# Optimization experiments

Measured on AMD Instinct MI355X. Metric: run time of the kernel, lower is better.

The kernel has to match this reference:

```python
import jax, jax.numpy as jnp
import numpy as np

N_NODES = 100000
N_EDGES = 1600000
IN_FEATS = 128
HIDDEN = 128
N_CLASSES = 47


def setup_inputs() -> dict:
    key = jax.random.key(0)
    ks = jax.random.split(key, 8)
    x = jax.random.normal(ks[0], (N_NODES, IN_FEATS), dtype=jnp.float32)
    edges = jax.random.randint(ks[1], (2, N_EDGES), 0, N_NODES, dtype=jnp.int32)
    W0 = jax.random.normal(ks[2], (IN_FEATS, HIDDEN), dtype=jnp.float32) * (1.0 / np.sqrt(IN_FEATS))
    b0 = jnp.zeros((HIDDEN,), dtype=jnp.float32)
    W1 = jax.random.normal(ks[3], (HIDDEN, HIDDEN), dtype=jnp.float32) * (1.0 / np.sqrt(HIDDEN))
    b1 = jnp.zeros((HIDDEN,), dtype=jnp.float32)
    Wc = jax.random.normal(ks[4], (HIDDEN, N_CLASSES), dtype=jnp.float32) * (1.0 / np.sqrt(HIDDEN))
    bc = jnp.zeros((N_CLASSES,), dtype=jnp.float32)
    return {"x": x, "edges": edges, "W0": W0, "b0": b0, "W1": W1, "b1": b1, "Wc": Wc, "bc": bc}


def reference(x, edges, W0, b0, W1, b1, Wc, bc):
    N = x.shape[0]
    src, dst = edges[0], edges[1]
    ones = jnp.ones((src.shape[0],), dtype=x.dtype)
    # symmetric 'both' normalization: out-degree for src, in-degree for dst (clamped to >=1)
    out_deg = jax.ops.segment_sum(ones, src, num_segments=N)
    in_deg = jax.ops.segment_sum(ones, dst, num_segments=N)
    c_src = jnp.maximum(out_deg, 1.0) ** -0.5  # [N]
    c_dst = jnp.maximum(in_deg, 1.0) ** -0.5   # [N]

    def graph_conv(h, W, b):
        h = (h * c_src[:, None]) @ W                       # dense transform [N, H]
        h = jax.ops.segment_sum(h[src], dst, num_segments=N)  # sparse SpMM aggregation
        h = h * c_dst[:, None] + b
        return jax.nn.relu(h)

    h = graph_conv(x, W0, b0)
    h = graph_conv(h, W1, b1)
    return h @ Wc + bc
```

## Files before the change

### kernel.cpp

```cpp
#include <hip/hip_runtime.h>
#include <hip/hip_fp16.h>


#define PB 256
#define BSHIFT 8

typedef _Float16 f16x8 __attribute__((ext_vector_type(8)));
typedef float f32x4 __attribute__((ext_vector_type(4)));


__global__ __launch_bounds__(256) void k_count(const int* __restrict__ src, const int* __restrict__ dst,
                                               int E, int per_blk, int NB,
                                               int* __restrict__ cntT, int* __restrict__ cntT2) {
  __shared__ int cnt[512];
  __shared__ int cnt2[512];
  for (int i = threadIdx.x; i < 512; i += 256) { cnt[i] = 0; cnt2[i] = 0; }
  __syncthreads();
  int e0 = blockIdx.x * per_blk, e1 = min(E, e0 + per_blk);
  for (int e = e0 + threadIdx.x; e < e1; e += 256) {
    atomicAdd(&cnt[dst[e] >> BSHIFT], 1);
    atomicAdd(&cnt2[src[e] >> BSHIFT], 1);
  }
  __syncthreads();
  for (int i = threadIdx.x; i < NB; i += 256) {
    cntT[i * PB + blockIdx.x] = cnt[i];
    cntT2[i * PB + blockIdx.x] = cnt2[i];
  }
}

__global__ __launch_bounds__(256) void k_scanblk(const int* __restrict__ cntT, int* __restrict__ offsT,
                                                 int* __restrict__ total) {
  __shared__ int s[256];
  int b = blockIdx.x, t = threadIdx.x;
  int v = cntT[b * PB + t];
  s[t] = v;
  __syncthreads();
  for (int off = 1; off < 256; off <<= 1) {
    int x = (t >= off) ? s[t - off] : 0;
    __syncthreads();
    s[t] += x;
    __syncthreads();
  }
  offsT[b * PB + t] = s[t] - v;
  if (t == 255) total[b] = s[255];
}

__global__ __launch_bounds__(512) void k_scantot(const int* __restrict__ total, int NB, int E,
                                                 int* __restrict__ bbase, int* __restrict__ sbase,
                                                 int* __restrict__ row_ptr, int N) {
  __shared__ int s[512];
  int t = threadIdx.x;
  const int* tot = (blockIdx.x == 0) ? total : total + NB;
  int* obase = (blockIdx.x == 0) ? bbase : sbase;
  int v = (t < NB) ? tot[t] : 0;
  s[t] = v;
  __syncthreads();
  for (int off = 1; off < 512; off <<= 1) {
    int x = (t >= off) ? s[t - off] : 0;
    __syncthreads();
    s[t] += x;
    __syncthreads();
  }
  if (t < NB) obase[t] = s[t] - v;
  if (t == 0) obase[NB] = E;
  if (blockIdx.x == 0 && t == 0) row_ptr[N] = E;
}


__global__ __launch_bounds__(256) void k_partition(const int* __restrict__ src, const int* __restrict__ dst,
                                                   int E, int per_blk, int NB,
                                                   const int* __restrict__ offsT, const int* __restrict__ bbase,
                                                   const int* __restrict__ offsT2, const int* __restrict__ sbase,
                                                   unsigned* __restrict__ ebuf, unsigned char* __restrict__ sbuf,
                                                   int src_bits) {
  __shared__ int cur[512];
  __shared__ int cur2[512];
  for (int i = threadIdx.x; i < NB; i += 256) {
    cur[i] = bbase[i] + offsT[i * PB + blockIdx.x];
    cur2[i] = sbase[i] + offsT2[i * PB + blockIdx.x];
  }
  __syncthreads();
  int e0 = blockIdx.x * per_blk, e1 = min(E, e0 + per_blk);
  for (int e = e0 + threadIdx.x; e < e1; e += 256) {
    int d = dst[e], s = src[e];
    int pos = atomicAdd(&cur[d >> BSHIFT], 1);
    ebuf[pos] = ((unsigned)(d & ((1 << BSHIFT) - 1)) << src_bits) | (unsigned)s;
    int pos2 = atomicAdd(&cur2[s >> BSHIFT], 1);
    sbuf[pos2] = (unsigned char)(s & ((1 << BSHIFT) - 1));
  }
}


__global__ __launch_bounds__(256) void k_finalize_src(const unsigned char* __restrict__ sbuf,
                                                      const int* __restrict__ sbase, int N,
                                                      float* __restrict__ c_src) {
  __shared__ int cnt[256];
  int b = blockIdx.x, t = threadIdx.x;
  cnt[t] = 0;
  __syncthreads();
  int q0 = sbase[b], q1 = sbase[b + 1];
  for (int i = q0 + t; i < q1; i += 256) atomicAdd(&cnt[sbuf[i]], 1);
  __syncthreads();
  int node = (b << BSHIFT) + t;
  if (node < N) c_src[node] = rsqrtf((float)max(cnt[t], 1));
}


__global__ __launch_bounds__(256) void k_fin_gemm(const unsigned* __restrict__ ebuf, const int* __restrict__ bbase,
                                                  int N, int src_bits, int NB,
                                                  int* __restrict__ row_ptr, float* __restrict__ c_dst,
                                                  int* __restrict__ col_idx,
                                                  const float* __restrict__ A, const float* __restrict__ W,
                                                  const float* __restrict__ scale, __half* __restrict__ out) {
  __shared__ _Float16 Wt[128][136];
  int t = threadIdx.x;

  if (blockIdx.x < NB) {
    int* cnt = (int*)&Wt[0][0];
    int* s = cnt + 256;
    int* cur = cnt + 512;
    int b = blockIdx.x;
    int r0 = bbase[b], r1 = bbase[b + 1];
    cnt[t] = 0;
    __syncthreads();
    for (int i = r0 + t; i < r1; i += 256) atomicAdd(&cnt[ebuf[i] >> src_bits], 1);
    __syncthreads();
    int v = cnt[t];
    s[t] = v;
    __syncthreads();
    for (int off = 1; off < 256; off <<= 1) {
      int x = (t >= off) ? s[t - off] : 0;
      __syncthreads();
      s[t] += x;
      __syncthreads();
    }
    int ex = s[t] - v;
    cur[t] = ex;
    int node = (b << BSHIFT) + t;
    if (node < N) {
      row_ptr[node] = r0 + ex;
      c_dst[node] = rsqrtf((float)max(v, 1));
    }
    __syncthreads();
    unsigned smask = (1u << src_bits) - 1u;
    for (int i = r0 + t; i < r1; i += 256) {
      unsigned e = ebuf[i];
      int pos = r0 + atomicAdd(&cur[e >> src_bits], 1);
      col_idx[pos] = (int)((e & smask) << 8);
    }
    return;
  }

  int bid = blockIdx.x - NB;
  {
    int nlow = t & 15;
    int kplow = t >> 4;
#pragma unroll
    for (int j = 0; j < 32; j++) {
      int n = nlow + 16 * (j & 7);
      int kp = kplow + 16 * (j >> 3);
      float w0 = W[(size_t)(2 * kp) * 128 + n];
      float w1 = W[(size_t)(2 * kp + 1) * 128 + n];
      __half2 h2 = __floats2half2_rn(w0, w1);
      *(__half2*)&Wt[n][2 * kp] = h2;
    }
  }
  __syncthreads();

  int wave = t >> 6;
  int lane = t & 63;
  int li = lane & 15;
  int q = lane >> 4;

#pragma unroll
  for (int s2 = 0; s2 < 2; s2++) {
    int m0 = (bid * 2 + s2) * 128 + wave * 32;
    if (m0 >= N) break;

    int mrow[2];
    float csc[2];
    bool mok[2];
    const float* arow[2];
#pragma unroll
    for (int s = 0; s < 2; s++) {
      mrow[s] = m0 + s * 16 + li;
      mok[s] = mrow[s] < N;
      csc[s] = mok[s] ? scale[mrow[s]] : 0.f;
      arow[s] = A + (size_t)(mok[s] ? mrow[s] : 0) * 128;
    }

    f32x4 acc[2][8];
#pragma unroll
    for (int s = 0; s < 2; s++)
#pragma unroll
      for (int nt = 0; nt < 8; nt++) acc[s][nt] = (f32x4){0.f, 0.f, 0.f, 0.f};

#pragma unroll
    for (int kc = 0; kc < 128; kc += 32) {
      f16x8 af[2];
#pragma unroll
      for (int s = 0; s < 2; s++) {
        float4 a0 = *(const float4*)(arow[s] + kc + q * 8);
        float4 a1 = *(const float4*)(arow[s] + kc + q * 8 + 4);
        f16x8 v;
        v[0] = (_Float16)(a0.x * csc[s]);
        v[1] = (_Float16)(a0.y * csc[s]);
        v[2] = (_Float16)(a0.z * csc[s]);
        v[3] = (_Float16)(a0.w * csc[s]);
        v[4] = (_Float16)(a1.x * csc[s]);
        v[5] = (_Float16)(a1.y * csc[s]);
        v[6] = (_Float16)(a1.z * csc[s]);
        v[7] = (_Float16)(a1.w * csc[s]);
        af[s] = v;
      }
#pragma unroll
      for (int nt = 0; nt < 8; nt++) {
        f16x8 wf = *(const f16x8*)&Wt[nt * 16 + li][kc + q * 8];
        acc[0][nt] = __builtin_amdgcn_mfma_f32_16x16x32_f16(wf, af[0], acc[0][nt], 0, 0, 0);
        acc[1][nt] = __builtin_amdgcn_mfma_f32_16x16x32_f16(wf, af[1], acc[1][nt], 0, 0, 0);
      }
    }

#pragma unroll
    for (int s = 0; s < 2; s++) {
      if (!mok[s]) continue;
      size_t rb = (size_t)mrow[s] * 128;
#pragma unroll
      for (int nt = 0; nt < 8; nt++) {
        __half2 p0 = __floats2half2_rn(acc[s][nt][0], acc[s][nt][1]);
        __half2 p1 = __floats2half2_rn(acc[s][nt][2], acc[s][nt][3]);
        uint2 qv;
        qv.x = *(unsigned*)&p0;
        qv.y = *(unsigned*)&p1;
        *(uint2*)&out[rb + nt * 16 + q * 4] = qv;
      }
    }
  }
}


__device__ __forceinline__ f16x8 load_af(const __half* arow, int off, float csc) {
  f16x8 v = *(const f16x8*)(arow + off);
  _Float16 c = (_Float16)csc;
#pragma unroll
  for (int j = 0; j < 8; j++) v[j] = v[j] * c;
  return v;
}

__global__ __launch_bounds__(256) void k_gemm_mfma_h(const __half* __restrict__ A, const float* __restrict__ W,
                                                     const float* __restrict__ scale, __half* __restrict__ out, int N) {
  __shared__ _Float16 Wt[128][136];
  int t = threadIdx.x;
  {
    int nlow = t & 15;
    int kplow = t >> 4;
#pragma unroll
    for (int j = 0; j < 32; j++) {
      int n = nlow + 16 * (j & 7);
      int kp = kplow + 16 * (j >> 3);
      float w0 = W[(size_t)(2 * kp) * 128 + n];
      float w1 = W[(size_t)(2 * kp + 1) * 128 + n];
      __half2 h2 = __floats2half2_rn(w0, w1);
      *(__half2*)&Wt[n][2 * kp] = h2;
    }
  }
  __syncthreads();

  int wave = t >> 6;
  int lane = t & 63;
  int li = lane & 15;
  int q = lane >> 4;

#pragma unroll
  for (int s2 = 0; s2 < 2; s2++) {
    int m0 = (blockIdx.x * 2 + s2) * 128 + wave * 32;
    if (m0 >= N) break;

    int mrow[2];
    float csc[2];
    bool mok[2];
    const __half* arow[2];
#pragma unroll
    for (int s = 0; s < 2; s++) {
      mrow[s] = m0 + s * 16 + li;
      mok[s] = mrow[s] < N;
      csc[s] = mok[s] ? scale[mrow[s]] : 0.f;
      arow[s] = A + (size_t)(mok[s] ? mrow[s] : 0) * 128;
    }

    f32x4 acc[2][8];
#pragma unroll
    for (int s = 0; s < 2; s++)
#pragma unroll
      for (int nt = 0; nt < 8; nt++) acc[s][nt] = (f32x4){0.f, 0.f, 0.f, 0.f};

#pragma unroll
    for (int kc = 0; kc < 128; kc += 32) {
      f16x8 af[2];
#pragma unroll
      for (int s = 0; s < 2; s++) af[s] = load_af(arow[s], kc + q * 8, csc[s]);
#pragma unroll
      for (int nt = 0; nt < 8; nt++) {
        f16x8 wf = *(const f16x8*)&Wt[nt * 16 + li][kc + q * 8];
        acc[0][nt] = __builtin_amdgcn_mfma_f32_16x16x32_f16(wf, af[0], acc[0][nt], 0, 0, 0);
        acc[1][nt] = __builtin_amdgcn_mfma_f32_16x16x32_f16(wf, af[1], acc[1][nt], 0, 0, 0);
      }
    }

#pragma unroll
    for (int s = 0; s < 2; s++) {
      if (!mok[s]) continue;
      size_t rb = (size_t)mrow[s] * 128;
#pragma unroll
      for (int nt = 0; nt < 8; nt++) {
        __half2 p0 = __floats2half2_rn(acc[s][nt][0], acc[s][nt][1]);
        __half2 p1 = __floats2half2_rn(acc[s][nt][2], acc[s][nt][3]);
        uint2 qv;
        qv.x = *(unsigned*)&p0;
        qv.y = *(unsigned*)&p1;
        *(uint2*)&out[rb + nt * 16 + q * 4] = qv;
      }
    }
  }
}


__device__ __forceinline__ void acc_pair(float4& a, uint2 qa, uint2 qb) {
  __half2 s0 = __hadd2(*(__half2*)&qa.x, *(__half2*)&qb.x);
  __half2 s1 = __hadd2(*(__half2*)&qa.y, *(__half2*)&qb.y);
  float2 f0 = __half22float2(s0);
  float2 f1 = __half22float2(s1);
  a.x += f0.x; a.y += f0.y; a.z += f1.x; a.w += f1.y;
}

__device__ __forceinline__ void acc_one(float4& a, uint2 q) {
  float2 f0 = __half22float2(*(__half2*)&q.x);
  float2 f1 = __half22float2(*(__half2*)&q.y);
  a.x += f0.x; a.y += f0.y; a.z += f1.x; a.w += f1.y;
}

__global__ __launch_bounds__(256) void k_aggregate_h(const __half* __restrict__ hin, const int* __restrict__ rp,
                                                     const int* __restrict__ ci, const float* __restrict__ c_dst,
                                                     const float* __restrict__ bias, __half* __restrict__ hout, int N) {
  int v = blockIdx.x * 4 + (threadIdx.x >> 6);
  if (v >= N) return;
  int half_id = (threadIdx.x >> 5) & 1;
  int f4 = (threadIdx.x & 31) * 4;
  const char* hb = (const char*)hin + f4 * 2;
  int p0 = rp[v], pe = rp[v + 1];
  int mid = p0 + ((pe - p0 + 1) >> 1);
  int p = half_id ? mid : p0;
  int pend = half_id ? pe : mid;
  float4 a0 = make_float4(0.f, 0.f, 0.f, 0.f);
  float4 a1 = make_float4(0.f, 0.f, 0.f, 0.f);
  float4 a2 = make_float4(0.f, 0.f, 0.f, 0.f);
  float4 a3 = make_float4(0.f, 0.f, 0.f, 0.f);
  for (; p + 7 < pend; p += 8) {
    int u0 = ci[p];
    int u1 = ci[p + 1];
    int u2 = ci[p + 2];
    int u3 = ci[p + 3];
    int u4 = ci[p + 4];
    int u5 = ci[p + 5];
    int u6 = ci[p + 6];
    int u7 = ci[p + 7];
    uint2 q0 = *(const uint2*)(hb + (size_t)(unsigned)u0);
    uint2 q1 = *(const uint2*)(hb + (size_t)(unsigned)u1);
    uint2 q2 = *(const uint2*)(hb + (size_t)(unsigned)u2);
    uint2 q3 = *(const uint2*)(hb + (size_t)(unsigned)u3);
    uint2 q4 = *(const uint2*)(hb + (size_t)(unsigned)u4);
    uint2 q5 = *(const uint2*)(hb + (size_t)(unsigned)u5);
    uint2 q6 = *(const uint2*)(hb + (size_t)(unsigned)u6);
    uint2 q7 = *(const uint2*)(hb + (size_t)(unsigned)u7);
    acc_pair(a0, q0, q1);
    acc_pair(a1, q2, q3);
    acc_pair(a2, q4, q5);
    acc_pair(a3, q6, q7);
  }
  for (; p + 1 < pend; p += 2) {
    int u0 = ci[p];
    int u1 = ci[p + 1];
    uint2 q0 = *(const uint2*)(hb + (size_t)(unsigned)u0);
    uint2 q1 = *(const uint2*)(hb + (size_t)(unsigned)u1);
    acc_pair(a0, q0, q1);
  }
  if (p < pend) {
    uint2 q = *(const uint2*)(hb + (size_t)(unsigned)ci[p]);
    acc_one(a0, q);
  }
  a0.x += a1.x; a0.y += a1.y; a0.z += a1.z; a0.w += a1.w;
  a2.x += a3.x; a2.y += a3.y; a2.z += a3.z; a2.w += a3.w;
  a0.x += a2.x; a0.y += a2.y; a0.z += a2.z; a0.w += a2.w;
  a0.x += __shfl_xor(a0.x, 32);
  a0.y += __shfl_xor(a0.y, 32);
  a0.z += __shfl_xor(a0.z, 32);
  a0.w += __shfl_xor(a0.w, 32);
  if (half_id == 0) {
    float cd = c_dst[v];
    float4 b = *(const float4*)&bias[f4];
    float4 o;
    o.x = fmaxf(fmaf(a0.x, cd, b.x), 0.f);
    o.y = fmaxf(fmaf(a0.y, cd, b.y), 0.f);
    o.z = fmaxf(fmaf(a0.z, cd, b.z), 0.f);
    o.w = fmaxf(fmaf(a0.w, cd, b.w), 0.f);
    __half2 p0h = __floats2half2_rn(o.x, o.y);
    __half2 p1h = __floats2half2_rn(o.z, o.w);
    uint2 qv;
    qv.x = *(unsigned*)&p0h;
    qv.y = *(unsigned*)&p1h;
    *(uint2*)&hout[(size_t)v * 128 + f4] = qv;
  }
}


__global__ __launch_bounds__(256) void k_classifier_mfma(const __half* __restrict__ h, const float* __restrict__ Wc,
                                                         const float* __restrict__ bc, float* __restrict__ out, int N) {
  __shared__ _Float16 Wt[96][136];
  __shared__ float bs[48];
  int t = threadIdx.x;
  if (t < 47) bs[t] = bc[t];
  if (t == 47) bs[47] = 0.f;
  for (int i = t; i < 48 * 128; i += 256) {
    int n = i >> 7, k = i & 127;
    float w = (n < 47) ? Wc[(size_t)k * 47 + n] : 0.f;
    _Float16 hi = (_Float16)w;
    Wt[n][k] = hi;
    Wt[n + 48][k] = (_Float16)(w - (float)hi);
  }
  __syncthreads();

  int wave = t >> 6;
  int lane = t & 63;
  int li = lane & 15;
  int q = lane >> 4;

#pragma unroll
  for (int s2 = 0; s2 < 2; s2++) {
    int m0 = (blockIdx.x * 2 + s2) * 128 + wave * 32;
    if (m0 >= N) break;

    int mrow[2];
    bool mok[2];
    const __half* arow[2];
#pragma unroll
    for (int s = 0; s < 2; s++) {
      mrow[s] = m0 + s * 16 + li;
      mok[s] = mrow[s] < N;
      arow[s] = h + (size_t)(mok[s] ? mrow[s] : 0) * 128;
    }

    f32x4 acc[2][3];
#pragma unroll
    for (int s = 0; s < 2; s++)
#pragma unroll
      for (int nt = 0; nt < 3; nt++) acc[s][nt] = (f32x4){0.f, 0.f, 0.f, 0.f};

#pragma unroll
    for (int kc = 0; kc < 128; kc += 32) {
      f16x8 af[2];
#pragma unroll
      for (int s = 0; s < 2; s++) af[s] = *(const f16x8*)(arow[s] + kc + q * 8);
#pragma unroll
      for (int nt = 0; nt < 3; nt++) {
        f16x8 whi = *(const f16x8*)&Wt[nt * 16 + li][kc + q * 8];
        f16x8 wlo = *(const f16x8*)&Wt[48 + nt * 16 + li][kc + q * 8];
        acc[0][nt] = __builtin_amdgcn_mfma_f32_16x16x32_f16(whi, af[0], acc[0][nt], 0, 0, 0);
        acc[1][nt] = __builtin_amdgcn_mfma_f32_16x16x32_f16(whi, af[1], acc[1][nt], 0, 0, 0);
        acc[0][nt] = __builtin_amdgcn_mfma_f32_16x16x32_f16(wlo, af[0], acc[0][nt], 0, 0, 0);
        acc[1][nt] = __builtin_amdgcn_mfma_f32_16x16x32_f16(wlo, af[1], acc[1][nt], 0, 0, 0);
      }
    }

#pragma unroll
    for (int s = 0; s < 2; s++) {
      if (!mok[s]) continue;
      size_t rb = (size_t)mrow[s] * 47;
#pragma unroll
      for (int nt = 0; nt < 3; nt++) {
#pragma unroll
        for (int j = 0; j < 4; j++) {
          int c = nt * 16 + q * 4 + j;
          if (c < 47) out[rb + c] = acc[s][nt][j] + bs[c];
        }
      }
    }
  }
}


extern "C" void kernel_launch(void* const* d_in, const int* in_sizes, int n_in,
                              void* d_out, int out_size, void* d_ws, size_t ws_size,
                              hipStream_t stream) {
  const float* x  = (const float*)d_in[0];
  const int* edges = (const int*)d_in[1];
  const float* W0 = (const float*)d_in[2];
  const float* b0 = (const float*)d_in[3];
  const float* W1 = (const float*)d_in[4];
  const float* b1 = (const float*)d_in[5];
  const float* Wc = (const float*)d_in[6];
  const float* bc = (const float*)d_in[7];
  float* out = (float*)d_out;

  int N = in_sizes[0] / 128;
  int E = in_sizes[1] / 2;
  const int* src = edges;
  const int* dst = edges + E;

  int NB = (N + ((1 << BSHIFT) - 1)) >> BSHIFT;
  int src_bits = 0;
  while ((1 << src_bits) < N) src_bits++;
  int per_blk = (E + PB - 1) / PB;

  char* base = (char*)d_ws;
  size_t off = 0;
  auto alloc = [&](size_t bytes) -> void* {
    void* p = base + off;
    off += (bytes + 255) & ~(size_t)255;
    return p;
  };
  float* c_src = (float*)alloc((size_t)N * 4);
  float* c_dst = (float*)alloc((size_t)N * 4);
  int* row_ptr = (int*)alloc((size_t)(N + 1) * 4);
  int* col_idx = (int*)alloc((size_t)E * 4);
  __half* h0h = (__half*)alloc((size_t)N * 128 * 2);
  __half* h1h = (__half*)alloc((size_t)N * 128 * 2);

  char* hb = (char*)h1h;
  unsigned* ebuf = (unsigned*)hb;            hb += (size_t)E * 4;
  unsigned char* sbuf = (unsigned char*)hb;  hb += ((size_t)E + 255) & ~(size_t)255;
  int* cntT = (int*)hb;                      hb += (size_t)2 * NB * PB * 4;
  int* offsT = (int*)hb;                     hb += (size_t)2 * NB * PB * 4;
  int* total = (int*)hb;                     hb += (size_t)2 * NB * 4;
  int* bbase = (int*)hb;                     hb += (size_t)(NB + 1) * 4;
  int* sbase = (int*)hb;                     hb += (size_t)(NB + 1) * 4;
  int* cntT2 = cntT + (size_t)NB * PB;
  int* offsT2 = offsT + (size_t)NB * PB;

  k_count<<<PB, 256, 0, stream>>>(src, dst, E, per_blk, NB, cntT, cntT2);
  k_scanblk<<<2 * NB, 256, 0, stream>>>(cntT, offsT, total);
  k_scantot<<<2, 512, 0, stream>>>(total, NB, E, bbase, sbase, row_ptr, N);
  k_partition<<<PB, 256, 0, stream>>>(src, dst, E, per_blk, NB, offsT, bbase, offsT2, sbase,
                                      ebuf, sbuf, src_bits);
  k_finalize_src<<<NB, 256, 0, stream>>>(sbuf, sbase, N, c_src);

  int strips = (N + 127) / 128;
  int gblocks = (strips + 1) / 2;
  k_fin_gemm<<<NB + gblocks, 256, 0, stream>>>(ebuf, bbase, N, src_bits, NB,
                                               row_ptr, c_dst, col_idx,
                                               x, W0, c_src, h0h);
  k_aggregate_h<<<(N + 3) / 4, 256, 0, stream>>>(h0h, row_ptr, col_idx, c_dst, b0, h1h, N);
  k_gemm_mfma_h<<<gblocks, 256, 0, stream>>>(h1h, W1, c_src, h0h, N);
  k_aggregate_h<<<(N + 3) / 4, 256, 0, stream>>>(h0h, row_ptr, col_idx, c_dst, b1, h1h, N);
  k_classifier_mfma<<<gblocks, 256, 0, stream>>>(h1h, Wc, bc, out, N);
}
```

Baseline: 344.6 us.

## Compute out-degree with global atomics instead of a second bucket partition

```diff
diff --git a/kernel.cpp b/kernel.cpp
--- a/kernel.cpp
+++ b/kernel.cpp
@@ -9,28 +9,31 @@
 typedef float f32x4 __attribute__((ext_vector_type(4)));
 
 
-__global__ __launch_bounds__(256) void k_count(const int* __restrict__ src, const int* __restrict__ dst,
-                                               int E, int per_blk, int NB,
-                                               int* __restrict__ cntT, int* __restrict__ cntT2) {
+__global__ __launch_bounds__(256) void k_degsrc(const int* __restrict__ src, int E, int per_blk, int N,
+                                                int* __restrict__ deg8) {
+  int e0 = blockIdx.x * per_blk, e1 = min(E, e0 + per_blk);
+  int* my = deg8 + (size_t)(blockIdx.x & 7) * N;
+  for (int e = e0 + threadIdx.x; e < e1; e += 256) atomicAdd(&my[src[e]], 1);
+}
+
+
+__global__ __launch_bounds__(256) void k_count(const int* __restrict__ dst, int E, int per_blk, int NB,
+                                               int* __restrict__ cntT) {
   __shared__ int cnt[512];
-  __shared__ int cnt2[512];
-  for (int i = threadIdx.x; i < 512; i += 256) { cnt[i] = 0; cnt2[i] = 0; }
+  for (int i = threadIdx.x; i < 512; i += 256) cnt[i] = 0;
   __syncthreads();
   int e0 = blockIdx.x * per_blk, e1 = min(E, e0 + per_blk);
-  for (int e = e0 + threadIdx.x; e < e1; e += 256) {
-    atomicAdd(&cnt[dst[e] >> BSHIFT], 1);
-    atomicAdd(&cnt2[src[e] >> BSHIFT], 1);
-  }
-  __syncthreads();
-  for (int i = threadIdx.x; i < NB; i += 256) {
-    cntT[i * PB + blockIdx.x] = cnt[i];
-    cntT2[i * PB + blockIdx.x] = cnt2[i];
-  }
+  for (int e = e0 + threadIdx.x; e < e1; e += 256) atomicAdd(&cnt[dst[e] >> BSHIFT], 1);
+  __syncthreads();
+  for (int i = threadIdx.x; i < NB; i += 256) cntT[i * PB + blockIdx.x] = cnt[i];
 }
 
 __global__ __launch_bounds__(256) void k_scanblk(const int* __restrict__ cntT, int* __restrict__ offsT,
-                                                 int* __restrict__ total) {
+                                                 int* __restrict__ total, int NB, int E,
+                                                 int* __restrict__ bbase, int* __restrict__ row_ptr, int N,
+                                                 int* __restrict__ done) {
   __shared__ int s[256];
+  __shared__ int amLast;
   int b = blockIdx.x, t = threadIdx.x;
   int v = cntT[b * PB + t];
   s[t] = v;
@@ -43,66 +46,60 @@
   }
   offsT[b * PB + t] = s[t] - v;
   if (t == 255) total[b] = s[255];
-}
-
-__global__ __launch_bounds__(512) void k_scantot(const int* __restrict__ total, int NB, int E,
-                                                 int* __restrict__ bbase, int* __restrict__ sbase,
-                                                 int* __restrict__ row_ptr, int N) {
-  __shared__ int s[512];
-  int t = threadIdx.x;
-  const int* tot = (blockIdx.x == 0) ? total : total + NB;
-  int* obase = (blockIdx.x == 0) ? bbase : sbase;
-  int v = (t < NB) ? tot[t] : 0;
-  s[t] = v;
-  __syncthreads();
-  for (int off = 1; off < 512; off <<= 1) {
-    int x = (t >= off) ? s[t - off] : 0;
-    __syncthreads();
-    s[t] += x;
-    __syncthreads();
-  }
-  if (t < NB) obase[t] = s[t] - v;
-  if (t == 0) obase[NB] = E;
-  if (blockIdx.x == 0 && t == 0) row_ptr[N] = E;
+  __threadfence();
+  if (t == 0) amLast = (atomicAdd(done, 1) == (int)gridDim.x - 1);
+  __syncthreads();
+  if (!amLast) return;
+  __threadfence();
+  int carry = 0;
+  for (int base0 = 0; base0 < NB; base0 += 256) {
+    int idx = base0 + t;
+    int tv = (idx < NB) ? total[idx] : 0;
+    s[t] = tv;
+    __syncthreads();
+    for (int off = 1; off < 256; off <<= 1) {
+      int x = (t >= off) ? s[t - off] : 0;
+      __syncthreads();
+      s[t] += x;
+      __syncthreads();
+    }
+    if (idx < NB) bbase[idx] = carry + s[t] - tv;
+    carry += s[255];
+    __syncthreads();
+  }
+  if (t == 0) {
+    bbase[NB] = E;
+    row_ptr[N] = E;
+  }
 }
 
 
 __global__ __launch_bounds__(256) void k_partition(const int* __restrict__ src, const int* __restrict__ dst,
                                                    int E, int per_blk, int NB,
                                                    const int* __restrict__ offsT, const int* __restrict__ bbase,
-                                                   const int* __restrict__ offsT2, const int* __restrict__ sbase,
-                                                   unsigned* __restrict__ ebuf, unsigned char* __restrict__ sbuf,
-                                                   int src_bits) {
+                                                   unsigned* __restrict__ ebuf, int src_bits,
+                                                   const int* __restrict__ deg8, float* __restrict__ c_src, int N) {
+  if (blockIdx.x >= PB) {
+    int rb = blockIdx.x - PB;
+    int nend = min(N, rb * 1024 + 1024);
+    for (int n = rb * 1024 + threadIdx.x; n < nend; n += 256) {
+      int s8 = 0;
+#pragma unroll
+      for (int p = 0; p < 8; p++) s8 += deg8[(size_t)p * N + n];
+      c_src[n] = rsqrtf((float)max(s8, 1));
+    }
+    return;
+  }
   __shared__ int cur[512];
-  __shared__ int cur2[512];
-  for (int i = threadIdx.x; i < NB; i += 256) {
+  for (int i = threadIdx.x; i < NB; i += 256)
     cur[i] = bbase[i] + offsT[i * PB + blockIdx.x];
-    cur2[i] = sbase[i] + offsT2[i * PB + blockIdx.x];
-  }
   __syncthreads();
   int e0 = blockIdx.x * per_blk, e1 = min(E, e0 + per_blk);
   for (int e = e0 + threadIdx.x; e < e1; e += 256) {
     int d = dst[e], s = src[e];
     int pos = atomicAdd(&cur[d >> BSHIFT], 1);
     ebuf[pos] = ((unsigned)(d & ((1 << BSHIFT) - 1)) << src_bits) | (unsigned)s;
-    int pos2 = atomicAdd(&cur2[s >> BSHIFT], 1);
-    sbuf[pos2] = (unsigned char)(s & ((1 << BSHIFT) - 1));
-  }
-}
-
-
-__global__ __launch_bounds__(256) void k_finalize_src(const unsigned char* __restrict__ sbuf,
-                                                      const int* __restrict__ sbase, int N,
-                                                      float* __restrict__ c_src) {
-  __shared__ int cnt[256];
-  int b = blockIdx.x, t = threadIdx.x;
-  cnt[t] = 0;
-  __syncthreads();
-  int q0 = sbase[b], q1 = sbase[b + 1];
-  for (int i = q0 + t; i < q1; i += 256) atomicAdd(&cnt[sbuf[i]], 1);
-  __syncthreads();
-  int node = (b << BSHIFT) + t;
-  if (node < N) c_src[node] = rsqrtf((float)max(cnt[t], 1));
+  }
 }
 
 
@@ -510,6 +507,7 @@
   int src_bits = 0;
   while ((1 << src_bits) < N) src_bits++;
   int per_blk = (E + PB - 1) / PB;
+  int per_blk_d = (E + 1023) / 1024;
 
   char* base = (char*)d_ws;
   size_t off = 0;
@@ -526,22 +524,21 @@
   __half* h1h = (__half*)alloc((size_t)N * 128 * 2);
 
   char* hb = (char*)h1h;
+  int* done = (int*)hb;                      hb += 256;
+  int* deg8 = (int*)hb;                      hb += (size_t)8 * N * 4;
   unsigned* ebuf = (unsigned*)hb;            hb += (size_t)E * 4;
-  unsigned char* sbuf = (unsigned char*)hb;  hb += ((size_t)E + 255) & ~(size_t)255;
-  int* cntT = (int*)hb;                      hb += (size_t)2 * NB * PB * 4;
-  int* offsT = (int*)hb;                     hb += (size_t)2 * NB * PB * 4;
-  int* total = (int*)hb;                     hb += (size_t)2 * NB * 4;
+  int* cntT = (int*)hb;                      hb += (size_t)NB * PB * 4;
+  int* offsT = (int*)hb;                     hb += (size_t)NB * PB * 4;
+  int* total = (int*)hb;                     hb += (size_t)NB * 4;
   int* bbase = (int*)hb;                     hb += (size_t)(NB + 1) * 4;
-  int* sbase = (int*)hb;                     hb += (size_t)(NB + 1) * 4;
-  int* cntT2 = cntT + (size_t)NB * PB;
-  int* offsT2 = offsT + (size_t)NB * PB;
-
-  k_count<<<PB, 256, 0, stream>>>(src, dst, E, per_blk, NB, cntT, cntT2);
-  k_scanblk<<<2 * NB, 256, 0, stream>>>(cntT, offsT, total);
-  k_scantot<<<2, 512, 0, stream>>>(total, NB, E, bbase, sbase, row_ptr, N);
-  k_partition<<<PB, 256, 0, stream>>>(src, dst, E, per_blk, NB, offsT, bbase, offsT2, sbase,
-                                      ebuf, sbuf, src_bits);
-  k_finalize_src<<<NB, 256, 0, stream>>>(sbuf, sbase, N, c_src);
+
+  hipMemsetAsync(done, 0, 256 + (size_t)8 * N * 4, stream);
+  k_degsrc<<<1024, 256, 0, stream>>>(src, E, per_blk_d, N, deg8);
+  k_count<<<PB, 256, 0, stream>>>(dst, E, per_blk, NB, cntT);
+  k_scanblk<<<NB, 256, 0, stream>>>(cntT, offsT, total, NB, E, bbase, row_ptr, N, done);
+  int cs_blocks = (N + 1023) / 1024;
+  k_partition<<<PB + cs_blocks, 256, 0, stream>>>(src, dst, E, per_blk, NB, offsT, bbase,
+                                                  ebuf, src_bits, deg8, c_src, N);
 
   int strips = (N + 127) / 128;
   int gblocks = (strips + 1) / 2;
```

Result: slower. 411.3 us (+19.4%).

## Fuse bucket count and scans into one kernel with atomic offsets and last-block scan

Applied to the files above, without the earlier changes.

```diff
diff --git a/kernel.cpp b/kernel.cpp
--- a/kernel.cpp
+++ b/kernel.cpp
@@ -9,61 +9,75 @@
 typedef float f32x4 __attribute__((ext_vector_type(4)));
 
 
-__global__ __launch_bounds__(256) void k_count(const int* __restrict__ src, const int* __restrict__ dst,
-                                               int E, int per_blk, int NB,
-                                               int* __restrict__ cntT, int* __restrict__ cntT2) {
-  __shared__ int cnt[512];
-  __shared__ int cnt2[512];
-  for (int i = threadIdx.x; i < 512; i += 256) { cnt[i] = 0; cnt2[i] = 0; }
-  __syncthreads();
-  int e0 = blockIdx.x * per_blk, e1 = min(E, e0 + per_blk);
-  for (int e = e0 + threadIdx.x; e < e1; e += 256) {
-    atomicAdd(&cnt[dst[e] >> BSHIFT], 1);
-    atomicAdd(&cnt2[src[e] >> BSHIFT], 1);
-  }
-  __syncthreads();
-  for (int i = threadIdx.x; i < NB; i += 256) {
-    cntT[i * PB + blockIdx.x] = cnt[i];
-    cntT2[i * PB + blockIdx.x] = cnt2[i];
-  }
-}
-
-__global__ __launch_bounds__(256) void k_scanblk(const int* __restrict__ cntT, int* __restrict__ offsT,
-                                                 int* __restrict__ total) {
-  __shared__ int s[256];
-  int b = blockIdx.x, t = threadIdx.x;
-  int v = cntT[b * PB + t];
-  s[t] = v;
-  __syncthreads();
-  for (int off = 1; off < 256; off <<= 1) {
-    int x = (t >= off) ? s[t - off] : 0;
-    __syncthreads();
-    s[t] += x;
-    __syncthreads();
-  }
-  offsT[b * PB + t] = s[t] - v;
-  if (t == 255) total[b] = s[255];
-}
-
-__global__ __launch_bounds__(512) void k_scantot(const int* __restrict__ total, int NB, int E,
-                                                 int* __restrict__ bbase, int* __restrict__ sbase,
-                                                 int* __restrict__ row_ptr, int N) {
-  __shared__ int s[512];
-  int t = threadIdx.x;
-  const int* tot = (blockIdx.x == 0) ? total : total + NB;
-  int* obase = (blockIdx.x == 0) ? bbase : sbase;
-  int v = (t < NB) ? tot[t] : 0;
-  s[t] = v;
-  __syncthreads();
-  for (int off = 1; off < 512; off <<= 1) {
-    int x = (t >= off) ? s[t - off] : 0;
-    __syncthreads();
-    s[t] += x;
-    __syncthreads();
-  }
-  if (t < NB) obase[t] = s[t] - v;
-  if (t == 0) obase[NB] = E;
-  if (blockIdx.x == 0 && t == 0) row_ptr[N] = E;
+__global__ __launch_bounds__(256) void k_count_res(const int* __restrict__ src, const int* __restrict__ dst,
+                                                   int E, int per_blk, int NB,
+                                                   int* __restrict__ offsT, int* __restrict__ offsT2,
+                                                   int* __restrict__ gtot, int* __restrict__ gtot2,
+                                                   int* __restrict__ bbase, int* __restrict__ sbase,
+                                                   int* __restrict__ row_ptr, int N, int* __restrict__ done) {
+  __shared__ int cnt[1024];
+  __shared__ int cnt2[1024];
+  __shared__ int amLast;
+  int t = threadIdx.x, b = blockIdx.x;
+  for (int i = t; i < 1024; i += 256) { cnt[i] = 0; cnt2[i] = 0; }
+  __syncthreads();
+  int w = (t >> 6) & 1;
+  int e0 = b * per_blk, e1 = min(E, e0 + per_blk);
+  for (int e = e0 + t; e < e1; e += 256) {
+    atomicAdd(&cnt[w * 512 + (dst[e] >> BSHIFT)], 1);
+    atomicAdd(&cnt2[w * 512 + (src[e] >> BSHIFT)], 1);
+  }
+  __syncthreads();
+  for (int i = t; i < NB; i += 256) {
+    int c = cnt[i] + cnt[512 + i];
+    offsT[i * PB + b] = atomicAdd(&gtot[i * 32], c);
+    int c2 = cnt2[i] + cnt2[512 + i];
+    offsT2[i * PB + b] = atomicAdd(&gtot2[i * 32], c2);
+  }
+  __threadfence();
+  __syncthreads();
+  if (t == 0) amLast = (atomicAdd(done, 1) == (int)gridDim.x - 1);
+  __syncthreads();
+  if (!amLast) return;
+  __threadfence();
+  int* s = cnt;
+  int carry = 0;
+  for (int base0 = 0; base0 < NB; base0 += 256) {
+    int idx = base0 + t;
+    int tv = (idx < NB) ? gtot[idx * 32] : 0;
+    s[t] = tv;
+    __syncthreads();
+    for (int off = 1; off < 256; off <<= 1) {
+      int x = (t >= off) ? s[t - off] : 0;
+      __syncthreads();
+      s[t] += x;
+      __syncthreads();
+    }
+    if (idx < NB) bbase[idx] = carry + s[t] - tv;
+    carry += s[255];
+    __syncthreads();
+  }
+  carry = 0;
+  for (int base0 = 0; base0 < NB; base0 += 256) {
+    int idx = base0 + t;
+    int tv = (idx < NB) ? gtot2[idx * 32] : 0;
+    s[t] = tv;
+    __syncthreads();
+    for (int off = 1; off < 256; off <<= 1) {
+      int x = (t >= off) ? s[t - off] : 0;
+      __syncthreads();
+      s[t] += x;
+      __syncthreads();
+    }
+    if (idx < NB) sbase[idx] = carry + s[t] - tv;
+    carry += s[255];
+    __syncthreads();
+  }
+  if (t == 0) {
+    bbase[NB] = E;
+    sbase[NB] = E;
+    row_ptr[N] = E;
+  }
 }
 
 
@@ -526,19 +540,20 @@
   __half* h1h = (__half*)alloc((size_t)N * 128 * 2);
 
   char* hb = (char*)h1h;
+  int* done = (int*)hb;                      hb += 256;
+  int* gtot = (int*)hb;                      hb += (size_t)NB * 32 * 4;
+  int* gtot2 = (int*)hb;                     hb += (size_t)NB * 32 * 4;
   unsigned* ebuf = (unsigned*)hb;            hb += (size_t)E * 4;
   unsigned char* sbuf = (unsigned char*)hb;  hb += ((size_t)E + 255) & ~(size_t)255;
-  int* cntT = (int*)hb;                      hb += (size_t)2 * NB * PB * 4;
-  int* offsT = (int*)hb;                     hb += (size_t)2 * NB * PB * 4;
-  int* total = (int*)hb;                     hb += (size_t)2 * NB * 4;
+  int* offsT = (int*)hb;                     hb += (size_t)NB * PB * 4;
+  int* offsT2 = (int*)hb;                    hb += (size_t)NB * PB * 4;
   int* bbase = (int*)hb;                     hb += (size_t)(NB + 1) * 4;
   int* sbase = (int*)hb;                     hb += (size_t)(NB + 1) * 4;
-  int* cntT2 = cntT + (size_t)NB * PB;
-  int* offsT2 = offsT + (size_t)NB * PB;
-
-  k_count<<<PB, 256, 0, stream>>>(src, dst, E, per_blk, NB, cntT, cntT2);
-  k_scanblk<<<2 * NB, 256, 0, stream>>>(cntT, offsT, total);
-  k_scantot<<<2, 512, 0, stream>>>(total, NB, E, bbase, sbase, row_ptr, N);
+
+  size_t zbytes = 256 + (size_t)2 * NB * 32 * 4;
+  hipMemsetAsync(done, 0, zbytes, stream);
+  k_count_res<<<PB, 256, 0, stream>>>(src, dst, E, per_blk, NB, offsT, offsT2, gtot, gtot2,
+                                      bbase, sbase, row_ptr, N, done);
   k_partition<<<PB, 256, 0, stream>>>(src, dst, E, per_blk, NB, offsT, bbase, offsT2, sbase,
                                       ebuf, sbuf, src_bits);
   k_finalize_src<<<NB, 256, 0, stream>>>(sbuf, sbase, N, c_src);
```

After: 384.1 us. 11.4% more time.
